# Optimization experiments

Measured on AMD Instinct MI355X. Metric: run time of the kernel, lower is better.

Reference implementation:

```python
import math
import jax, jax.numpy as jnp
import numpy as np

B, S, D, H = 4, 1024, 1024, 16
HD = D // H
EPS = 1e-5


def _sinusoidal_encodings(length, d):
    pos = jnp.arange(length, dtype=jnp.float32)
    inv_freq = 1.0 / (10000.0 ** (jnp.arange(0.0, d, 2.0) / d))
    angles = pos[:, None] * inv_freq[None, :]  # [L, D/2]
    enc = jnp.zeros((length, d), dtype=jnp.float32)
    enc = enc.at[:, 0::2].set(jnp.sin(angles))
    enc = enc.at[:, 1::2].set(jnp.cos(angles))
    return enc


def _relative_shift(emb):
    # emb: [B, H, L, L] -- Transformer-XL shift trick
    b, h, l1, l2 = emb.shape
    padded = jnp.concatenate([jnp.zeros((b, h, l1, 1), emb.dtype), emb], axis=-1)
    padded = padded.reshape(b, h, l2 + 1, l1)
    return padded[:, :, 1:, :].reshape(b, h, l1, l2)


def setup_inputs() -> dict:
    key = jax.random.key(0)
    ks = jax.random.split(key, 12)
    s = 0.02
    inp = {
        "x": jax.random.normal(ks[0], (B, S, D), dtype=jnp.float32),
        "Wq": jax.random.normal(ks[1], (D, D), dtype=jnp.float32) * s,
        "bq": jnp.zeros((D,), jnp.float32),
        "Wk": jax.random.normal(ks[2], (D, D), dtype=jnp.float32) * s,
        "bk": jnp.zeros((D,), jnp.float32),
        "Wv": jax.random.normal(ks[3], (D, D), dtype=jnp.float32) * s,
        "bv": jnp.zeros((D,), jnp.float32),
        "Wpos": jax.random.normal(ks[4], (D, D), dtype=jnp.float32) * s,
        "Wf": jax.random.normal(ks[5], (D, D), dtype=jnp.float32) * s,
        "bf": jnp.zeros((D,), jnp.float32),
        "u": jax.random.normal(ks[6], (H, HD), dtype=jnp.float32) * s,
        "v": jax.random.normal(ks[7], (H, HD), dtype=jnp.float32) * s,
        "gamma": jnp.ones((D,), jnp.float32),
        "beta": jnp.zeros((D,), jnp.float32),
    }
    return inp


def reference(x, Wq, bq, Wk, bk, Wv, bv, Wpos, Wf, bf, u, v, gamma, beta):
    b, s, d = x.shape
    # LayerNorm
    mu = jnp.mean(x, axis=-1, keepdims=True)
    var = jnp.mean((x - mu) ** 2, axis=-1, keepdims=True)
    xn = (x - mu) * jax.lax.rsqrt(var + EPS) * gamma + beta

    pe = _sinusoidal_encodings(s, d)  # [S, D]

    q = (xn @ Wq + bq).reshape(b, s, H, HD)
    k = (xn @ Wk + bk).reshape(b, s, H, HD)
    val = (xn @ Wv + bv).reshape(b, s, H, HD)
    p = (pe @ Wpos).reshape(s, H, HD)

    # content-content and content-position scores
    AC = jnp.einsum("bihd,bjhd->bhij", q + u, k)
    BD = jnp.einsum("bihd,jhd->bhij", q + v, p)
    BD = _relative_shift(BD)

    attn = jax.nn.softmax((AC + BD) / math.sqrt(d), axis=-1)  # [B,H,S,S]
    out = jnp.einsum("bhij,bjhd->bihd", attn, val).reshape(b, s, d)
    out = out @ Wf + bf  # dropout is identity (p=0 / eval)
    return out
```

## Files before the change

### kernel.cpp

```cpp
#include <hip/hip_runtime.h>
#include <math.h>


typedef __bf16 bf16;
typedef __bf16 bf16x8 __attribute__((ext_vector_type(8)));
typedef __bf16 bf16x4 __attribute__((ext_vector_type(4)));
typedef float f32x4 __attribute__((ext_vector_type(4)));

#define S_ 1024
#define D_ 1024
#define PROWS 3136
#define POFF 1088

#define AS1 __attribute__((address_space(1)))
#define AS3 __attribute__((address_space(3)))

static __device__ __forceinline__ f32x4 mfma16(bf16x8 a, bf16x8 b, f32x4 c) {
  return __builtin_amdgcn_mfma_f32_16x16x32_bf16(a, b, c, 0, 0, 0);
}

static constexpr size_t OXN  = 0;
static constexpr size_t OWTQ = OXN  + (size_t)4096*1024*2;
static constexpr size_t OWTK = OWTQ + (size_t)1024*1024*2;
static constexpr size_t OWTV = OWTK + (size_t)1024*1024*2;
static constexpr size_t OWTP = OWTV + (size_t)1024*1024*2;
static constexpr size_t OWTF = OWTP + (size_t)1024*1024*2;
static constexpr size_t OPE  = OWTF + (size_t)1024*1024*2;
static constexpr size_t OQU  = OPE  + (size_t)1024*1024*2;
static constexpr size_t OQV  = OQU  + (size_t)64*1024*64*2;
static constexpr size_t OKB  = OQV  + (size_t)64*1024*64*2 + 256;
static constexpr size_t OVT  = OKB  + (size_t)64*1024*64*2;
static constexpr size_t OPP  = OVT  + (size_t)64*1024*64*2;
static constexpr size_t PPBYTES = (size_t)16*PROWS*64*2;
static constexpr size_t OOB  = OPP  + PPBYTES;
static constexpr size_t OBU  = OOB  + (size_t)4096*1024*2;
static constexpr size_t OBV2 = OBU  + 4096;

__global__ __launch_bounds__(256) void prep_kernel(
    const float* __restrict__ x, const float* __restrict__ gamma,
    const float* __restrict__ beta, bf16* __restrict__ xn,
    const float* __restrict__ W0, const float* __restrict__ W1,
    const float* __restrict__ W2, const float* __restrict__ W3,
    const float* __restrict__ W4, bf16* __restrict__ outbase,
    const float* __restrict__ bq, const float* __restrict__ u,
    const float* __restrict__ v, float* __restrict__ bu, float* __restrict__ bv2,
    bf16* __restrict__ pe, uint4* __restrict__ pz) {
  int blk = blockIdx.x, t = threadIdx.x;
  __shared__ float tile[32][33];
  __shared__ float red[8];
  if (blk < 4096) {
    int row = blk;
    const float4* xr = (const float4*)(x + (size_t)row * D_);
    float4 vv = xr[t];
    float s  = vv.x + vv.y + vv.z + vv.w;
    float ss = vv.x*vv.x + vv.y*vv.y + vv.z*vv.z + vv.w*vv.w;
    for (int off = 32; off; off >>= 1) {
      s  += __shfl_xor(s, off);
      ss += __shfl_xor(ss, off);
    }
    int wid = t >> 6;
    if ((t & 63) == 0) { red[wid] = s; red[wid + 4] = ss; }
    __syncthreads();
    float S  = red[0] + red[1] + red[2] + red[3];
    float SS = red[4] + red[5] + red[6] + red[7];
    float mu = S * (1.f / 1024.f);
    float rstd = rsqrtf(SS * (1.f / 1024.f) - mu * mu + 1e-5f);
    float4 g  = ((const float4*)gamma)[t];
    float4 bb = ((const float4*)beta)[t];
    bf16x4 o;
    o[0] = (bf16)((vv.x - mu) * rstd * g.x + bb.x);
    o[1] = (bf16)((vv.y - mu) * rstd * g.y + bb.y);
    o[2] = (bf16)((vv.z - mu) * rstd * g.z + bb.z);
    o[3] = (bf16)((vv.w - mu) * rstd * g.w + bb.w);
    *(bf16x4*)(xn + (size_t)row * D_ + t * 4) = o;
  } else if (blk < 9216) {
    int idx = blk - 4096;
    int z = idx >> 10, rem = idx & 1023;
    int bx = rem & 31, by = rem >> 5;
    const float* W = z == 0 ? W0 : z == 1 ? W1 : z == 2 ? W2 : z == 3 ? W3 : W4;
    bf16* WT = outbase + (size_t)z * 1024 * 1024;
    int tx = t & 31, ty = t >> 5;
    #pragma unroll
    for (int i = 0; i < 4; i++)
      tile[ty + i * 8][tx] = W[(size_t)(by * 32 + ty + i * 8) * D_ + bx * 32 + tx];
    __syncthreads();
    #pragma unroll
    for (int i = 0; i < 4; i++)
      WT[(size_t)(bx * 32 + ty + i * 8) * D_ + by * 32 + tx] = (bf16)tile[tx][ty + i * 8];
  } else {
    int mblk = blk - 9216;
    if (mblk < 1024) {
      int pos = mblk;
      #pragma unroll
      for (int pp = 0; pp < 2; pp++) {
        int f = t + pp * 256;
        float inv = expf(-(2.0f * (float)f * (1.0f / 1024.0f)) * 9.210340371976184f);
        float ang = (float)pos * inv;
        pe[(size_t)pos * D_ + 2 * f]     = (bf16)sinf(ang);
        pe[(size_t)pos * D_ + 2 * f + 1] = (bf16)cosf(ang);
      }
    } else if (mblk < 1024 + 1568) {
      int i = (mblk - 1024) * 256 + t;
      pz[i] = make_uint4(0u, 0u, 0u, 0u);
    } else {
      int c = (mblk - 2592) * 256 + t;
      if (c < 1024) { bu[c] = bq[c] + u[c]; bv2[c] = bq[c] + v[c]; }
    }
  }
}

__global__ __launch_bounds__(256) void gemm_qkvp_kernel(
    const bf16* __restrict__ xn, const bf16* __restrict__ pe,
    const bf16* __restrict__ BT,
    const float* __restrict__ bu, const float* __restrict__ bv2,
    const float* __restrict__ bk, const float* __restrict__ bv,
    bf16* __restrict__ quB, bf16* __restrict__ qvB,
    bf16* __restrict__ kbB, bf16* __restrict__ vtB, bf16* __restrict__ ppd) {
  __shared__ __align__(16) bf16 As[128 * 32];
  __shared__ __align__(16) bf16 Bs[128 * 32];
  int lin = blockIdx.x;
  int swz = (lin & 7) * 104 + (lin >> 3);
  int m0, n0, sect;
  const bf16* Abase;
  int nrow0;
  if (swz < 768) {
    int bx = swz % 24, by = swz / 24;
    m0 = by * 128; n0 = bx * 128;
    sect = n0 >> 10;
    Abase = xn; nrow0 = n0;
  } else {
    int pp = swz - 768;
    int bx = pp & 7, by = pp >> 3;
    m0 = by * 128; n0 = bx * 128;
    sect = 3;
    Abase = pe; nrow0 = 3072 + n0;
  }
  int t = threadIdx.x, l = t & 63, w = t >> 6;
  int lr = l & 15, lq = l >> 4;
  int wr = w >> 1, wc = w & 1;
  f32x4 acc[4][4];
  #pragma unroll
  for (int mi = 0; mi < 4; mi++)
    #pragma unroll
    for (int ni = 0; ni < 4; ni++) acc[mi][ni] = (f32x4){0.f, 0.f, 0.f, 0.f};
  int srow = l >> 2, scol = (l & 3) * 8;
  for (int kk = 0; kk < 1024; kk += 32) {
    #pragma unroll
    for (int c2 = 0; c2 < 2; c2++) {
      int ch = w * 2 + c2;
      const bf16* ga = Abase + (size_t)(m0 + ch * 16 + srow) * 1024 + kk + scol;
      __builtin_amdgcn_global_load_lds((const AS1 void*)ga, (AS3 void*)(As + ch * 512), 16, 0, 0);
      const bf16* gb = BT + (size_t)(nrow0 + ch * 16 + srow) * 1024 + kk + scol;
      __builtin_amdgcn_global_load_lds((const AS1 void*)gb, (AS3 void*)(Bs + ch * 512), 16, 0, 0);
    }
    __syncthreads();
    bf16x8 af[4], bfv[4];
    #pragma unroll
    for (int mi = 0; mi < 4; mi++)
      af[mi] = *(const bf16x8*)(As + (wr * 64 + mi * 16 + lr) * 32 + lq * 8);
    #pragma unroll
    for (int ni = 0; ni < 4; ni++)
      bfv[ni] = *(const bf16x8*)(Bs + (wc * 64 + ni * 16 + lr) * 32 + lq * 8);
    if (sect == 2) {
      #pragma unroll
      for (int mi = 0; mi < 4; mi++)
        #pragma unroll
        for (int ni = 0; ni < 4; ni++)
          acc[mi][ni] = mfma16(bfv[ni], af[mi], acc[mi][ni]);
    } else {
      #pragma unroll
      for (int mi = 0; mi < 4; mi++)
        #pragma unroll
        for (int ni = 0; ni < 4; ni++)
          acc[mi][ni] = mfma16(af[mi], bfv[ni], acc[mi][ni]);
    }
    __syncthreads();
  }
  if (sect == 2) {
    #pragma unroll
    for (int mi = 0; mi < 4; mi++)
      #pragma unroll
      for (int ni = 0; ni < 4; ni++)
        #pragma unroll
        for (int rr = 0; rr < 4; rr++) {
          int wcol = (n0 - 2048) + wc * 64 + ni * 16 + lq * 4 + rr;
          int srw  = m0 + wr * 64 + mi * 16 + lr;
          int b = srw >> 10, s = srw & 1023, h = wcol >> 6, hd = wcol & 63;
          vtB[(((size_t)(b * 16 + h)) * 64 + hd) * 1024 + s] =
              (bf16)(acc[mi][ni][rr] + bv[wcol]);
        }
  } else if (sect == 3) {
    #pragma unroll
    for (int mi = 0; mi < 4; mi++)
      #pragma unroll
      for (int ni = 0; ni < 4; ni++)
        #pragma unroll
        for (int rr = 0; rr < 4; rr++) {
          int row = m0 + wr * 64 + mi * 16 + lq * 4 + rr;
          int col = n0 + wc * 64 + ni * 16 + lr;
          int h = col >> 6, hd = col & 63;
          ppd[((size_t)h * PROWS + POFF + row) * 64 + hd] = (bf16)acc[mi][ni][rr];
        }
  } else {
    #pragma unroll
    for (int mi = 0; mi < 4; mi++)
      #pragma unroll
      for (int ni = 0; ni < 4; ni++)
        #pragma unroll
        for (int rr = 0; rr < 4; rr++) {
          int row = m0 + wr * 64 + mi * 16 + lq * 4 + rr;
          int col = n0 + wc * 64 + ni * 16 + lr;
          float vv = acc[mi][ni][rr];
          int b = row >> 10, s = row & 1023;
          if (sect == 0) {
            int h = col >> 6, hd = col & 63;
            size_t idx = (((size_t)(b * 16 + h)) * 1024 + s) * 64 + hd;
            quB[idx] = (bf16)(vv + bu[col]);
            qvB[idx] = (bf16)(vv + bv2[col]);
          } else {
            int c = col - 1024, h = c >> 6, hd = c & 63;
            size_t idx = (((size_t)(b * 16 + h)) * 1024 + s) * 64 + hd;
            kbB[idx] = (bf16)(vv + bk[c]);
          }
        }
  }
}

__global__ __launch_bounds__(256) void gemm_final_kernel(
    const bf16* __restrict__ A, const bf16* __restrict__ BT,
    const float* __restrict__ bias0, float* __restrict__ out0) {
  __shared__ __align__(16) bf16 As[128 * 32];
  __shared__ __align__(16) bf16 Bs[128 * 32];
  int gx = gridDim.x;
  int lin = blockIdx.x + gx * blockIdx.y;
  int cpx = (gx * gridDim.y) >> 3;
  int swz = (lin & 7) * cpx + (lin >> 3);
  int bx = swz % gx, by = swz / gx;
  int m0 = by * 128, n0 = bx * 128;
  int t = threadIdx.x, l = t & 63, w = t >> 6;
  int lr = l & 15, lq = l >> 4;
  int wr = w >> 1, wc = w & 1;
  f32x4 acc[4][4];
  #pragma unroll
  for (int mi = 0; mi < 4; mi++)
    #pragma unroll
    for (int ni = 0; ni < 4; ni++) acc[mi][ni] = (f32x4){0.f, 0.f, 0.f, 0.f};
  int srow = l >> 2, scol = (l & 3) * 8;
  for (int kk = 0; kk < 1024; kk += 32) {
    #pragma unroll
    for (int c2 = 0; c2 < 2; c2++) {
      int ch = w * 2 + c2;
      const bf16* ga = A + (size_t)(m0 + ch * 16 + srow) * 1024 + kk + scol;
      __builtin_amdgcn_global_load_lds((const AS1 void*)ga, (AS3 void*)(As + ch * 512), 16, 0, 0);
      const bf16* gb = BT + (size_t)(n0 + ch * 16 + srow) * 1024 + kk + scol;
      __builtin_amdgcn_global_load_lds((const AS1 void*)gb, (AS3 void*)(Bs + ch * 512), 16, 0, 0);
    }
    __syncthreads();
    bf16x8 af[4], bfv[4];
    #pragma unroll
    for (int mi = 0; mi < 4; mi++)
      af[mi] = *(const bf16x8*)(As + (wr * 64 + mi * 16 + lr) * 32 + lq * 8);
    #pragma unroll
    for (int ni = 0; ni < 4; ni++)
      bfv[ni] = *(const bf16x8*)(Bs + (wc * 64 + ni * 16 + lr) * 32 + lq * 8);
    #pragma unroll
    for (int mi = 0; mi < 4; mi++)
      #pragma unroll
      for (int ni = 0; ni < 4; ni++)
        acc[mi][ni] = mfma16(af[mi], bfv[ni], acc[mi][ni]);
    __syncthreads();
  }
  #pragma unroll
  for (int mi = 0; mi < 4; mi++)
    #pragma unroll
    for (int ni = 0; ni < 4; ni++)
      #pragma unroll
      for (int rr = 0; rr < 4; rr++) {
        int row = m0 + wr * 64 + mi * 16 + lq * 4 + rr;
        int col = n0 + wc * 64 + ni * 16 + lr;
        out0[(size_t)row * 1024 + col] = acc[mi][ni][rr] + bias0[col];
      }
}

__global__ __launch_bounds__(256) void attn_kernel(
    const bf16* __restrict__ qu, const bf16* __restrict__ qv,
    const bf16* __restrict__ kb, const bf16* __restrict__ vt,
    const bf16* __restrict__ ppad, bf16* __restrict__ ob) {
  int bid = blockIdx.x;
  int xcd = bid & 7, slot = bid >> 3;
  int g = slot >> 4, qblk = slot & 15;
  int bh = xcd + 8 * g;
  int h = bh & 15, b = bh >> 4;

  int t = threadIdx.x, l = t & 63, wid = t >> 6;
  int lr = l & 15, lq = l >> 4;
  int w0 = qblk * 64 + wid * 16;
  const bf16* quB = qu + (size_t)bh * S_ * 64;
  const bf16* qvB = qv + (size_t)bh * S_ * 64;
  const char* kBy = (const char*)(kb + (size_t)bh * S_ * 64);
  const char* vBy = (const char*)(vt + (size_t)bh * 64 * S_);
  const bf16* pH  = ppad + (size_t)h * PROWS * 64;

  __shared__ __align__(16) bf16 Kbuf[2][4096];
  __shared__ __align__(16) bf16 Vbuf[2][4096];
  __shared__ __align__(16) bf16 G1s[4][16][84];
  __shared__ __align__(16) bf16 G2s[4][16][84];
  bf16* PlW = &G1s[wid][0][0];

  bf16x8 aqu[2], aqv1[2], aqv2[2];
  #pragma unroll
  for (int ks = 0; ks < 2; ks++) {
    aqu[ks]  = *(const bf16x8*)(quB + (size_t)(w0 + lr) * 64 + ks * 32 + lq * 8);
    aqv1[ks] = *(const bf16x8*)(qvB + (size_t)(w0 + lr) * 64 + ks * 32 + lq * 8);
    aqv2[ks] = *(const bf16x8*)(qvB + (size_t)(w0 + 1 + lr) * 64 + ks * 32 + lq * 8);
  }
  bf16x8 ones;
  #pragma unroll
  for (int e = 0; e < 8; e++) ones[e] = (bf16)1.0f;

  float m_run[4];
  f32x4 accL = (f32x4){0.f, 0.f, 0.f, 0.f};
  f32x4 accO[4];
  #pragma unroll
  for (int rr = 0; rr < 4; rr++) m_run[rr] = -1e30f;
  #pragma unroll
  for (int nf = 0; nf < 4; nf++) accO[nf] = (f32x4){0.f, 0.f, 0.f, 0.f};

  const float SC = 0.045084220f;

  int srow8 = l >> 3;
  int scolb = (l & 7) * 16;
  auto stage = [&](int nb, int j0n) {
    #pragma unroll
    for (int ci = 0; ci < 4; ci++) {
      int c = wid * 4 + ci;
      int cc = c & 7;
      int row = cc * 8 + srow8;
      int colsrc = scolb ^ ((row & 7) << 4);
      if (c < 8) {
        const char* src = kBy + (size_t)(j0n + row) * 128 + colsrc;
        __builtin_amdgcn_global_load_lds((const AS1 void*)src,
            (AS3 void*)(&Kbuf[nb][cc * 512]), 16, 0, 0);
      } else {
        const char* src = vBy + (size_t)row * 2048 + j0n * 2 + colsrc;
        __builtin_amdgcn_global_load_lds((const AS1 void*)src,
            (AS3 void*)(&Vbuf[nb][cc * 512]), 16, 0, 0);
      }
    }
  };

  stage(0, 0);
  __syncthreads();

  for (int tt = 0; tt < 16; tt++) {
    int j0 = tt * 64;
    int cur = tt & 1;
    if (tt < 15) stage(cur ^ 1, j0 + 64);

    const char* Ks = (const char*)&Kbuf[cur][0];
    const char* Vs = (const char*)&Vbuf[cur][0];
    int d = w0 - j0;

    f32x4 accS[4];
    __builtin_amdgcn_s_setprio(1);
    #pragma unroll
    for (int nf = 0; nf < 4; nf++) {
      accS[nf] = (f32x4){0.f, 0.f, 0.f, 0.f};
      int rowk = nf * 16 + lr;
      #pragma unroll
      for (int ks = 0; ks < 2; ks++) {
        int off = ((rowk << 7) + (ks << 6) + (lq << 4)) ^ ((rowk & 7) << 4);
        bf16x8 bk8 = *(const bf16x8*)(Ks + off);
        accS[nf] = mfma16(aqu[ks], bk8, accS[nf]);
      }
    }
    __builtin_amdgcn_s_setprio(0);

    if (d >= 63) {
      int pb = 1023 - w0 + j0 - 15 + POFF;
      bf16x8 bp[10];
      #pragma unroll
      for (int gf = 0; gf < 5; gf++)
        #pragma unroll
        for (int ks = 0; ks < 2; ks++)
          bp[gf * 2 + ks] = *(const bf16x8*)(pH + (size_t)(pb + gf * 16 + lr) * 64 + ks * 32 + lq * 8);
      #pragma unroll
      for (int gf = 0; gf < 5; gf++) {
        f32x4 gg = (f32x4){0.f, 0.f, 0.f, 0.f};
        gg = mfma16(aqv1[0], bp[gf * 2 + 0], gg);
        gg = mfma16(aqv1[1], bp[gf * 2 + 1], gg);
        #pragma unroll
        for (int rr = 0; rr < 4; rr++) G1s[wid][lq * 4 + rr][gf * 16 + lr] = (bf16)gg[rr];
      }
    } else if (d <= -17) {
      int pb = j0 - w0 - 17 + POFF;
      bf16x8 bp[10];
      #pragma unroll
      for (int gf = 0; gf < 5; gf++)
        #pragma unroll
        for (int ks = 0; ks < 2; ks++)
          bp[gf * 2 + ks] = *(const bf16x8*)(pH + (size_t)(pb + gf * 16 + lr) * 64 + ks * 32 + lq * 8);
      #pragma unroll
      for (int gf = 0; gf < 5; gf++) {
        f32x4 gg = (f32x4){0.f, 0.f, 0.f, 0.f};
        gg = mfma16(aqv2[0], bp[gf * 2 + 0], gg);
        gg = mfma16(aqv2[1], bp[gf * 2 + 1], gg);
        #pragma unroll
        for (int rr = 0; rr < 4; rr++) G2s[wid][lq * 4 + rr][gf * 16 + lr] = (bf16)gg[rr];
      }
    } else {
      {
        int pb = 1023 - w0 + j0 - 15 + POFF;
        int gmax = (d + 15) >> 4; if (gmax > 4) gmax = 4;
        for (int gf = 0; gf <= gmax; gf++) {
          f32x4 gg = (f32x4){0.f, 0.f, 0.f, 0.f};
          #pragma unroll
          for (int ks = 0; ks < 2; ks++) {
            bf16x8 bp = *(const bf16x8*)(pH + (size_t)(pb + gf * 16 + lr) * 64 + ks * 32 + lq * 8);
            gg = mfma16(aqv1[ks], bp, gg);
          }
          #pragma unroll
          for (int rr = 0; rr < 4; rr++) G1s[wid][lq * 4 + rr][gf * 16 + lr] = (bf16)gg[rr];
        }
      }
      {
        int pb = j0 - w0 - 17 + POFF;
        int t2 = d + 17;
        int gmin = t2 > 0 ? (t2 >> 4) : 0;
        for (int gf = gmin; gf < 5; gf++) {
          f32x4 gg = (f32x4){0.f, 0.f, 0.f, 0.f};
          #pragma unroll
          for (int ks = 0; ks < 2; ks++) {
            bf16x8 bp = *(const bf16x8*)(pH + (size_t)(pb + gf * 16 + lr) * 64 + ks * 32 + lq * 8);
            gg = mfma16(aqv2[ks], bp, gg);
          }
          #pragma unroll
          for (int rr = 0; rr < 4; rr++) G2s[wid][lq * 4 + rr][gf * 16 + lr] = (bf16)gg[rr];
        }
      }
    }

    float sc[4][4];
    if (d >= 63) {
      #pragma unroll
      for (int nf = 0; nf < 4; nf++)
        #pragma unroll
        for (int rr = 0; rr < 4; rr++) {
          int ii = lq * 4 + rr;
          int u = nf * 16 + lr - ii + 15;
          sc[nf][rr] = (accS[nf][rr] + (float)G1s[wid][ii][u]) * SC;
        }
    } else if (d <= -17) {
      #pragma unroll
      for (int nf = 0; nf < 4; nf++)
        #pragma unroll
        for (int rr = 0; rr < 4; rr++) {
          int ii = lq * 4 + rr;
          int u = nf * 16 + lr - ii + 15;
          sc[nf][rr] = (accS[nf][rr] + (float)G2s[wid][ii][u]) * SC;
        }
    } else {
      #pragma unroll
      for (int nf = 0; nf < 4; nf++)
        #pragma unroll
        for (int rr = 0; rr < 4; rr++) {
          int ii = lq * 4 + rr;
          int jj = nf * 16 + lr;
          int dd = jj - ii;
          int u = dd + 15;
          float g1v = (float)G1s[wid][ii][u];
          float g2v = (float)G2s[wid][ii][u];
          float bd = dd <= d ? g1v : (dd == d + 1 ? 0.f : g2v);
          sc[nf][rr] = (accS[nf][rr] + bd) * SC;
        }
    }

    float lmax[4];
    #pragma unroll
    for (int rr = 0; rr < 4; rr++)
      lmax[rr] = fmaxf(fmaxf(sc[0][rr], sc[1][rr]), fmaxf(sc[2][rr], sc[3][rr]));
    bool ok = (lmax[0] <= m_run[0] + 8.f) && (lmax[1] <= m_run[1] + 8.f) &&
              (lmax[2] <= m_run[2] + 8.f) && (lmax[3] <= m_run[3] + 8.f);
    if (!__all((int)ok)) {
      float rmax[4];
      #pragma unroll
      for (int rr = 0; rr < 4; rr++) rmax[rr] = lmax[rr];
      #pragma unroll
      for (int st = 1; st < 16; st <<= 1)
        #pragma unroll
        for (int rr = 0; rr < 4; rr++) rmax[rr] = fmaxf(rmax[rr], __shfl_xor(rmax[rr], st));
      #pragma unroll
      for (int rr = 0; rr < 4; rr++) {
        float mnew = fmaxf(m_run[rr], rmax[rr]);
        float sv = exp2f(m_run[rr] - mnew);
        m_run[rr] = mnew;
        accL[rr] *= sv;
        #pragma unroll
        for (int nf = 0; nf < 4; nf++) accO[nf][rr] *= sv;
      }
    }

    #pragma unroll
    for (int nf = 0; nf < 4; nf++)
      #pragma unroll
      for (int rr = 0; rr < 4; rr++) {
        float p = exp2f(sc[nf][rr] - m_run[rr]);
        PlW[(lq * 4 + rr) * 72 + nf * 16 + lr] = (bf16)p;
      }

    bf16x8 ap[2];
    #pragma unroll
    for (int ks = 0; ks < 2; ks++)
      ap[ks] = *(const bf16x8*)(PlW + lr * 72 + ks * 32 + lq * 8);
    __builtin_amdgcn_s_setprio(1);
    #pragma unroll
    for (int ks = 0; ks < 2; ks++) accL = mfma16(ap[ks], ones, accL);
    #pragma unroll
    for (int nf = 0; nf < 4; nf++) {
      int rowd = nf * 16 + lr;
      #pragma unroll
      for (int ks = 0; ks < 2; ks++) {
        int off = ((rowd << 7) + (ks << 6) + (lq << 4)) ^ ((rowd & 7) << 4);
        bf16x8 bv8 = *(const bf16x8*)(Vs + off);
        accO[nf] = mfma16(ap[ks], bv8, accO[nf]);
      }
    }
    __builtin_amdgcn_s_setprio(0);

    __syncthreads();
  }

  #pragma unroll
  for (int nf = 0; nf < 4; nf++)
    #pragma unroll
    for (int rr = 0; rr < 4; rr++) {
      int i = w0 + lq * 4 + rr;
      float o = accO[nf][rr] / accL[rr];
      ob[((size_t)(b * S_ + i)) * 1024 + h * 64 + nf * 16 + lr] = (bf16)o;
    }
}

extern "C" void kernel_launch(void* const* d_in, const int* in_sizes, int n_in,
                              void* d_out, int out_size, void* d_ws, size_t ws_size,
                              hipStream_t stream) {
  const float* x     = (const float*)d_in[0];
  const float* Wq    = (const float*)d_in[1];
  const float* bq    = (const float*)d_in[2];
  const float* Wk    = (const float*)d_in[3];
  const float* bk    = (const float*)d_in[4];
  const float* Wv    = (const float*)d_in[5];
  const float* bv    = (const float*)d_in[6];
  const float* Wpos  = (const float*)d_in[7];
  const float* Wf    = (const float*)d_in[8];
  const float* bf_   = (const float*)d_in[9];
  const float* u     = (const float*)d_in[10];
  const float* v     = (const float*)d_in[11];
  const float* gamma = (const float*)d_in[12];
  const float* beta  = (const float*)d_in[13];

  char* ws = (char*)d_ws;
  bf16* xn  = (bf16*)(ws + OXN);
  bf16* wtq = (bf16*)(ws + OWTQ);
  bf16* wtf = (bf16*)(ws + OWTF);
  bf16* pe  = (bf16*)(ws + OPE);
  bf16* quB = (bf16*)(ws + OQU);
  bf16* qvB = (bf16*)(ws + OQV);
  bf16* kbB = (bf16*)(ws + OKB);
  bf16* vtB = (bf16*)(ws + OVT);
  bf16* ppd = (bf16*)(ws + OPP);
  bf16* obB = (bf16*)(ws + OOB);
  float* bu  = (float*)(ws + OBU);
  float* bv2 = (float*)(ws + OBV2);

  prep_kernel<<<11812, 256, 0, stream>>>(x, gamma, beta, xn,
                                         Wq, Wk, Wv, Wpos, Wf, wtq,
                                         bq, u, v, bu, bv2, pe, (uint4*)(ws + OPP));

  gemm_qkvp_kernel<<<832, 256, 0, stream>>>(xn, pe, wtq, bu, bv2, bk, bv,
                                            quB, qvB, kbB, vtB, ppd);

  attn_kernel<<<1024, 256, 0, stream>>>(quB, qvB, kbB, vtB, ppd, obB);

  gemm_final_kernel<<<dim3(8, 32), 256, 0, stream>>>(obB, wtf, bf_, (float*)d_out);
}
```

Before: 251.3 us.

## Prefetch next tile's positional window into registers with double-buffered arrays

Loads the positional-embedding window for the next key tile into registers during the current tile, ping-ponging two register arrays via a 2x-unrolled loop lambda. This hides global-load latency of the Wpos window behind softmax and PV math. It also sets launch_bounds occupancy to 2 waves-groups per CU, which may cap registers and cause spills given the extra 20 bf16x8 registers held live.

Result: faster. 235.5 us (median of 2 runs) (-6.3%).

```diff
diff --git a/kernel.cpp b/kernel.cpp
--- a/kernel.cpp
+++ b/kernel.cpp
@@ -282,7 +282,7 @@
       }
 }
 
-__global__ __launch_bounds__(256) void attn_kernel(
+__global__ __launch_bounds__(256, 2) void attn_kernel(
     const bf16* __restrict__ qu, const bf16* __restrict__ qv,
     const bf16* __restrict__ kb, const bf16* __restrict__ vt,
     const bf16* __restrict__ ppad, bf16* __restrict__ ob) {
@@ -349,10 +349,20 @@
     }
   };
 
+  bf16x8 bpA[10], bpB[10];
+  auto loadwin = [&](bf16x8 (&bp)[10], int pb) {
+    #pragma unroll
+    for (int gf = 0; gf < 5; gf++)
+      #pragma unroll
+      for (int ks = 0; ks < 2; ks++)
+        bp[gf * 2 + ks] = *(const bf16x8*)(pH + (size_t)(pb + gf * 16 + lr) * 64 + ks * 32 + lq * 8);
+  };
+
   stage(0, 0);
+  if (w0 >= 63) loadwin(bpA, 1023 - w0 - 15 + POFF);
   __syncthreads();
 
-  for (int tt = 0; tt < 16; tt++) {
+  auto tile = [&](int tt, bf16x8 (&bpC)[10], bf16x8 (&bpN)[10]) {
     int j0 = tt * 64;
     int cur = tt & 1;
     if (tt < 15) stage(cur ^ 1, j0 + 64);
@@ -377,34 +387,20 @@
     __builtin_amdgcn_s_setprio(0);
 
     if (d >= 63) {
-      int pb = 1023 - w0 + j0 - 15 + POFF;
-      bf16x8 bp[10];
-      #pragma unroll
-      for (int gf = 0; gf < 5; gf++)
-        #pragma unroll
-        for (int ks = 0; ks < 2; ks++)
-          bp[gf * 2 + ks] = *(const bf16x8*)(pH + (size_t)(pb + gf * 16 + lr) * 64 + ks * 32 + lq * 8);
       #pragma unroll
       for (int gf = 0; gf < 5; gf++) {
         f32x4 gg = (f32x4){0.f, 0.f, 0.f, 0.f};
-        gg = mfma16(aqv1[0], bp[gf * 2 + 0], gg);
-        gg = mfma16(aqv1[1], bp[gf * 2 + 1], gg);
+        gg = mfma16(aqv1[0], bpC[gf * 2 + 0], gg);
+        gg = mfma16(aqv1[1], bpC[gf * 2 + 1], gg);
         #pragma unroll
         for (int rr = 0; rr < 4; rr++) G1s[wid][lq * 4 + rr][gf * 16 + lr] = (bf16)gg[rr];
       }
     } else if (d <= -17) {
-      int pb = j0 - w0 - 17 + POFF;
-      bf16x8 bp[10];
-      #pragma unroll
-      for (int gf = 0; gf < 5; gf++)
-        #pragma unroll
-        for (int ks = 0; ks < 2; ks++)
-          bp[gf * 2 + ks] = *(const bf16x8*)(pH + (size_t)(pb + gf * 16 + lr) * 64 + ks * 32 + lq * 8);
       #pragma unroll
       for (int gf = 0; gf < 5; gf++) {
         f32x4 gg = (f32x4){0.f, 0.f, 0.f, 0.f};
-        gg = mfma16(aqv2[0], bp[gf * 2 + 0], gg);
-        gg = mfma16(aqv2[1], bp[gf * 2 + 1], gg);
+        gg = mfma16(aqv2[0], bpC[gf * 2 + 0], gg);
+        gg = mfma16(aqv2[1], bpC[gf * 2 + 1], gg);
         #pragma unroll
         for (int rr = 0; rr < 4; rr++) G2s[wid][lq * 4 + rr][gf * 16 + lr] = (bf16)gg[rr];
       }
@@ -440,6 +436,13 @@
       }
     }
 
+    if (tt < 15) {
+      int dn = d - 64;
+      int j0n = j0 + 64;
+      if (dn >= 63)       loadwin(bpN, 1023 - w0 + j0n - 15 + POFF);
+      else if (dn <= -17) loadwin(bpN, j0n - w0 - 17 + POFF);
+    }
+
     float sc[4][4];
     if (d >= 63) {
       #pragma unroll
@@ -528,6 +531,12 @@
     __builtin_amdgcn_s_setprio(0);
 
     __syncthreads();
+  };
+
+  #pragma unroll 1
+  for (int tt = 0; tt < 16; tt += 2) {
+    tile(tt,     bpA, bpB);
+    tile(tt + 1, bpB, bpA);
   }
 
   #pragma unroll
```
